# Optimization experiments

Measured on AMD Instinct MI355X. Metric: run time of the kernel, lower is better.

## Reference

```python
import jax, jax.numpy as jnp
import numpy as np

TOP_K = 128
HID = 256


def _mlp2(h, w1, b1, w2, b2):
    return jax.nn.relu(h @ w1 + b1) @ w2 + b2


def setup_inputs() -> dict:
    key = jax.random.key(0)
    ks = jax.random.split(key, 20)
    B, L, D = 512, 256, 64
    s = 0.05
    inp = {
        "x": jax.random.normal(ks[0], (B, L, D), dtype=jnp.float32),
        "Wq": jax.random.normal(ks[1], (D, HID)) * s, "bq": jnp.zeros((HID,)),
        "Wk": jax.random.normal(ks[2], (D, HID)) * s, "bk": jnp.zeros((HID,)),
        "phi_w1": jax.random.normal(ks[3], (D, HID)) * s, "phi_b1": jnp.zeros((HID,)),
        "phi_w2": jax.random.normal(ks[4], (HID, HID)) * s, "phi_b2": jnp.zeros((HID,)),
        "xi_w1": jax.random.normal(ks[5], (2 * D, HID)) * s, "xi_b1": jnp.zeros((HID,)),
        "xi_w2": jax.random.normal(ks[6], (HID, HID)) * s, "xi_b2": jnp.zeros((HID,)),
        "rho_w1": jax.random.normal(ks[7], (HID, HID)) * s, "rho_b1": jnp.zeros((HID,)),
        "rho_w2": jax.random.normal(ks[8], (HID, 128)) * s, "rho_b2": jnp.zeros((128,)),
    }
    return inp


def reference(x, Wq, bq, Wk, bk, phi_w1, phi_b1, phi_w2, phi_b2,
              xi_w1, xi_b1, xi_w2, xi_b2, rho_w1, rho_b1, rho_w2, rho_b2):
    B, L, D = x.shape
    scale = HID ** (-0.5)
    # padding mask (all True for randn input; trim is identity with static shapes)
    pad = jnp.sum(jnp.abs(x), axis=-1) != 0  # [B, L]
    Q = x @ Wq + bq  # [B, L, H]
    K = x @ Wk + bk
    scores = jnp.einsum("blh,bmh->blm", Q, K) * scale  # [B, L, L]
    mask2d = pad[:, :, None] & pad[:, None, :]
    scores = jnp.where(mask2d, scores, -jnp.inf)
    flat = scores.reshape(B, L * L)
    k = min(TOP_K, L * L)
    topk_vals, topk_idx = jax.lax.top_k(flat, k)  # [B, k]
    topk_w = jax.nn.softmax(topk_vals, axis=-1)
    row = topk_idx // L
    col = topk_idx % L
    x_i = jnp.take_along_axis(x, row[:, :, None], axis=1)  # [B, k, D]
    x_j = jnp.take_along_axis(x, col[:, :, None], axis=1)
    feat_self = _mlp2(x_i, phi_w1, phi_b1, phi_w2, phi_b2)  # [B, k, H]
    feat_pair = _mlp2(jnp.concatenate([x_i, x_j], axis=-1), xi_w1, xi_b1, xi_w2, xi_b2)
    self_mask = (row == col)[:, :, None]
    interaction = jnp.where(self_mask, feat_self, feat_pair)
    pooled = jnp.sum(interaction * topk_w[:, :, None], axis=1)  # [B, H]
    return _mlp2(pooled, rho_w1, rho_b1, rho_w2, rho_b2)  # [B, 128]
```

## Files before the change

kernel.cpp:

```cpp
#include <hip/hip_runtime.h>

typedef unsigned short u16;
typedef unsigned int   u32;
typedef unsigned char  u8;
typedef unsigned long long u64;

#define B_TOT 512
#define L_SEQ 256
#define D_IN  64
#define HIDN  256
#define TOPK  128
#define CAP   160
#define NWT   32
#define FLDS  113280

typedef float  f32x4  __attribute__((ext_vector_type(4)));
typedef __bf16 bf16x8 __attribute__((ext_vector_type(8)));

__device__ __forceinline__ u16 f2bf(float f){
  u32 u = __float_as_uint(f);
  u32 r = u + 0x7fffu + ((u>>16)&1u);
  return (u16)(r>>16);
}
__device__ __forceinline__ u32 sortKey(float f){
  u32 b = __float_as_uint(f);
  return (b & 0x80000000u) ? ~b : (b | 0x80000000u);
}
__device__ __forceinline__ float unKey(u32 u){
  u32 b = (u & 0x80000000u) ? (u & 0x7fffffffu) : ~u;
  return __uint_as_float(b);
}
__device__ __forceinline__ void cvt8(const float* v, u32* hp, u32* lp){
  #pragma unroll
  for (int i=0;i<4;++i){
    float v0 = v[2*i], v1 = v[2*i+1];
    u16 h0 = f2bf(v0); float h0f = __uint_as_float(((u32)h0)<<16); u16 l0 = f2bf(v0 - h0f);
    u16 h1 = f2bf(v1); float h1f = __uint_as_float(((u32)h1)<<16); u16 l1 = f2bf(v1 - h1f);
    hp[i] = (u32)h0 | ((u32)h1<<16);
    lp[i] = (u32)l0 | ((u32)l1<<16);
  }
}

__global__ __launch_bounds__(256) void k_wprep(
    const float* __restrict__ Wq, const float* __restrict__ bq,
    const float* __restrict__ Wk, const float* __restrict__ bk,
    const float* __restrict__ xi_w1, const float* __restrict__ phi_w1,
    u16* __restrict__ MtH, u16* __restrict__ MtL, float* __restrict__ uvc,
    u16* __restrict__ xiH, u16* __restrict__ xiL,
    u16* __restrict__ phiH, u16* __restrict__ phiL)
{
  int bid = blockIdx.x, tid = threadIdx.x;
  if (bid < 64){
    __shared__ float wq[HIDN];
    __shared__ float part[256];
    int a = bid;
    wq[tid] = Wq[a*HIDN + tid];
    __syncthreads();
    int bcol = tid & 63, q = tid >> 6;
    float s = 0.f;
    for (int h = q*64; h < q*64 + 64; ++h)
      s = fmaf(wq[h], Wk[bcol*HIDN + h], s);
    part[tid] = s;
    __syncthreads();
    if (tid < 64){
      float mv = part[tid] + part[64+tid] + part[128+tid] + part[192+tid];
      u16 hh = f2bf(mv); float hf = __uint_as_float(((u32)hh)<<16);
      u16 ll = f2bf(mv - hf);
      MtH[tid*64 + a] = hh;
      MtL[tid*64 + a] = ll;
    }
    int wv = tid >> 6, ln = tid & 63;
    if (wv == 0){
      float s2 = 0.f;
      #pragma unroll
      for (int i=0;i<4;++i){ int h = ln*4+i; s2 = fmaf(wq[h], bk[h], s2); }
      #pragma unroll
      for (int off=1; off<64; off<<=1) s2 += __shfl_xor(s2, off);
      if (ln == 0) uvc[a] = s2;
    } else if (wv == 1){
      float s2 = 0.f;
      #pragma unroll
      for (int i=0;i<4;++i){ int h = ln*4+i; s2 = fmaf(Wk[a*HIDN + h], bq[h], s2); }
      #pragma unroll
      for (int off=1; off<64; off<<=1) s2 += __shfl_xor(s2, off);
      if (ln == 0) uvc[64 + a] = s2;
    } else if (wv == 2 && a == 0){
      float s2 = 0.f;
      #pragma unroll
      for (int i=0;i<4;++i){ int h = ln*4+i; s2 = fmaf(bq[h], bk[h], s2); }
      #pragma unroll
      for (int off=1; off<64; off<<=1) s2 += __shfl_xor(s2, off);
      if (ln == 0) uvc[128] = s2;
    }
  } else {
    int t = (bid-64)*256 + tid;
    if (t < 256*128){
      int h = t >> 7, d = t & 127;
      float v = xi_w1[d*HIDN + h];
      u16 hh = f2bf(v); float hf = __uint_as_float(((u32)hh)<<16);
      u16 ll = f2bf(v - hf);
      xiH[h*128 + d] = hh; xiL[h*128 + d] = ll;
    } else {
      int t2 = t - 256*128;
      int h = t2 >> 6, d = t2 & 63;
      float v = phi_w1[d*HIDN + h];
      u16 hh = f2bf(v); float hf = __uint_as_float(((u32)hh)<<16);
      u16 ll = f2bf(v - hf);
      phiH[h*64 + d] = hh; phiL[h*64 + d] = ll;
    }
  }
}

__global__ __launch_bounds__(512) void k_fused(
    const float* __restrict__ x, const u16* __restrict__ MtH, const u16* __restrict__ MtL,
    const float* __restrict__ uvc,
    u64* __restrict__ cand, int* __restrict__ cand_n, u32* __restrict__ uthr)
{
  extern __shared__ __align__(16) u16 smem[];
  u16* XH = smem;
  u16* XL = XH + 256*72;
  u16* YH = XL + 256*72;
  u16* YL = YH + 128*72;
  float* STS = (float*)(YL + 128*72);
  float* STT = STS + 256;
  float* SUV = STT + 256;

  int tid = threadIdx.x;
  int b = blockIdx.x;
  const float* xb = x + (size_t)b*(L_SEQ*D_IN);

  if (tid < 129) SUV[tid] = uvc[tid];

  int ar = tid >> 1, ahf = tid & 1;
  float v[32];
  {
    const float* src = xb + (size_t)ar*D_IN + ahf*32;
    #pragma unroll
    for (int i=0;i<8;++i) *(float4*)&v[i*4] = *(const float4*)(src + i*4);
    u32 hp[16], lp[16];
    cvt8(&v[0],  &hp[0],  &lp[0]);
    cvt8(&v[8],  &hp[4],  &lp[4]);
    cvt8(&v[16], &hp[8],  &lp[8]);
    cvt8(&v[24], &hp[12], &lp[12]);
    u16* dh = XH + ar*72 + ahf*32;
    u16* dl = XL + ar*72 + ahf*32;
    #pragma unroll
    for (int i=0;i<4;++i){
      *(uint4*)(dh + i*8) = make_uint4(hp[i*4],hp[i*4+1],hp[i*4+2],hp[i*4+3]);
      *(uint4*)(dl + i*8) = make_uint4(lp[i*4],lp[i*4+1],lp[i*4+2],lp[i*4+3]);
    }
  }
  __syncthreads();

  {
    float pA=0.f, pB=0.f, qA=0.f, qB=0.f, pa=0.f;
    #pragma unroll
    for (int d=0; d<16; ++d){
      float xa = v[d];
      pA = fmaf(xa, SUV[ahf*32+d], pA);
      qA = fmaf(xa, SUV[64+ahf*32+d], qA);
      pa += fabsf(xa);
    }
    #pragma unroll
    for (int d=16; d<32; ++d){
      float xa = v[d];
      pB = fmaf(xa, SUV[ahf*32+d], pB);
      qB = fmaf(xa, SUV[64+ahf*32+d], qB);
      pa += fabsf(xa);
    }
    float su = pA + pB, tv = qA + qB;
    su += __shfl_xor(su,1); tv += __shfl_xor(tv,1); pa += __shfl_xor(pa,1);
    if (ahf == 0){
      bool pad = (pa != 0.f);
      STS[ar] = pad ? (su + SUV[128]) : -1e38f;
      STT[ar] = pad ? tv : -1e38f;
    }
  }
  __syncthreads();

  int w = tid >> 6, lane = tid & 63, lm = lane & 15, quad = lane >> 4;

  for (int half=0; half<2; ++half){
    int u = w + 8*half;
    int r0 = u*16;

    {
      const u16* ah = XH + (r0+lm)*72;
      const u16* al = XL + (r0+lm)*72;
      bf16x8 Ah0 = *(const bf16x8*)(ah + quad*8);
      bf16x8 Ah1 = *(const bf16x8*)(ah + 32 + quad*8);
      bf16x8 Al0 = *(const bf16x8*)(al + quad*8);
      bf16x8 Al1 = *(const bf16x8*)(al + 32 + quad*8);
      #pragma unroll
      for (int ct=0; ct<4; ++ct){
        const u16* mth = MtH + (ct*16+lm)*64 + quad*8;
        const u16* mtl = MtL + (ct*16+lm)*64 + quad*8;
        bf16x8 Bh0 = *(const bf16x8*)(mth);
        bf16x8 Bh1 = *(const bf16x8*)(mth + 32);
        bf16x8 Bl0 = *(const bf16x8*)(mtl);
        bf16x8 Bl1 = *(const bf16x8*)(mtl + 32);
        f32x4 a1 = {0.f,0.f,0.f,0.f}, a2 = {0.f,0.f,0.f,0.f};
        a1 = __builtin_amdgcn_mfma_f32_16x16x32_bf16(Ah0, Bh0, a1, 0,0,0);
        a2 = __builtin_amdgcn_mfma_f32_16x16x32_bf16(Ah1, Bh1, a2, 0,0,0);
        a1 = __builtin_amdgcn_mfma_f32_16x16x32_bf16(Al0, Bh0, a1, 0,0,0);
        a2 = __builtin_amdgcn_mfma_f32_16x16x32_bf16(Al1, Bh1, a2, 0,0,0);
        a1 = __builtin_amdgcn_mfma_f32_16x16x32_bf16(Ah0, Bl0, a1, 0,0,0);
        a2 = __builtin_amdgcn_mfma_f32_16x16x32_bf16(Ah1, Bl1, a2, 0,0,0);
        #pragma unroll
        for (int rg=0; rg<4; ++rg){
          float vy = a1[rg] + a2[rg];
          u16 hh = f2bf(vy); float hf = __uint_as_float(((u32)hh)<<16);
          u16 ll = f2bf(vy - hf);
          YH[(w*16 + quad*4 + rg)*72 + ct*16 + lm] = hh;
          YL[(w*16 + quad*4 + rg)*72 + ct*16 + lm] = ll;
        }
      }
    }
    const u16* yh_ = YH + (w*16+lm)*72;
    const u16* yl_ = YL + (w*16+lm)*72;
    bf16x8 Yh0 = *(const bf16x8*)(yh_ + quad*8);
    bf16x8 Yh1 = *(const bf16x8*)(yh_ + 32 + quad*8);
    bf16x8 Yl0 = *(const bf16x8*)(yl_ + quad*8);
    bf16x8 Yl1 = *(const bf16x8*)(yl_ + 32 + quad*8);

    float sr[4];
    #pragma unroll
    for (int r=0;r<4;++r) sr[r] = STS[r0 + quad*4 + r];

    for (int ch=0; ch<2; ++ch){
      int j0 = ch*128;
      u32 kv[32];
      #pragma unroll
      for (int ct=0; ct<8; ++ct){
        const u16* bh = XH + (j0 + ct*16+lm)*72;
        const u16* bl = XL + (j0 + ct*16+lm)*72;
        bf16x8 Bh0 = *(const bf16x8*)(bh + quad*8);
        bf16x8 Bh1 = *(const bf16x8*)(bh + 32 + quad*8);
        bf16x8 Bl0 = *(const bf16x8*)(bl + quad*8);
        bf16x8 Bl1 = *(const bf16x8*)(bl + 32 + quad*8);
        f32x4 a1 = {0.f,0.f,0.f,0.f}, a2 = {0.f,0.f,0.f,0.f};
        a1 = __builtin_amdgcn_mfma_f32_16x16x32_bf16(Yh0, Bh0, a1, 0,0,0);
        a2 = __builtin_amdgcn_mfma_f32_16x16x32_bf16(Yh1, Bh1, a2, 0,0,0);
        a1 = __builtin_amdgcn_mfma_f32_16x16x32_bf16(Yl0, Bh0, a1, 0,0,0);
        a2 = __builtin_amdgcn_mfma_f32_16x16x32_bf16(Yl1, Bh1, a2, 0,0,0);
        a1 = __builtin_amdgcn_mfma_f32_16x16x32_bf16(Yh0, Bl0, a1, 0,0,0);
        a2 = __builtin_amdgcn_mfma_f32_16x16x32_bf16(Yh1, Bl1, a2, 0,0,0);
        float tc = STT[j0 + ct*16 + lm];
        #pragma unroll
        for (int r=0;r<4;++r)
          kv[ct*4 + r] = sortKey(a1[r] + a2[r] + sr[r] + tc);
      }

      u32 T = 0;
      for (int bit=15; bit>=0; --bit){
        u32 th2 = (T | (1u<<bit)) << 16;
        int c0 = 0, c1 = 0;
        #pragma unroll
        for (int i=0;i<32;i+=2){
          c0 += (int)__popcll(__ballot(kv[i]   >= th2));
          c1 += (int)__popcll(__ballot(kv[i+1] >= th2));
        }
        int c = c0 + c1;
        if (c >= TOPK){
          T |= (1u<<bit);
          if (c <= CAP) break;
        }
      }
      u32 thr = T << 16;
      u32 up  = (T < 0xffffu) ? ((T+1u) << 16) : 0xffffffffu;

      u32 m1 = 0, m2 = 0;
      #pragma unroll
      for (int i=0;i<32;++i){
        bool ge = kv[i] >= thr;
        bool c1 = ge && (kv[i] >= up);
        m1 |= (c1 ? 1u : 0u) << i;
        m2 |= ((ge && !c1) ? 1u : 0u) << i;
      }
      int n1 = __popc(m1), n2 = __popc(m2);
      int p1 = n1, p2 = n2;
      #pragma unroll
      for (int off=1; off<64; off<<=1){
        int a = __shfl_up(p1, off); if (lane >= off) p1 += a;
        int c = __shfl_up(p2, off); if (lane >= off) p2 += c;
      }
      int tot1 = __shfl(p1, 63), tot2 = __shfl(p2, 63);
      int pos1 = p1 - n1;
      int pos2 = tot1 + (p2 - n2);
      int total = tot1 + tot2;
      int wt = u*2 + ch;
      size_t base = ((size_t)b*NWT + wt)*CAP;
      if (lane == 0){
        cand_n[b*NWT + wt] = (total < CAP) ? total : CAP;
        uthr[b*NWT + wt] = thr;
      }
      {
        int o1=0, o2=0;
        #pragma unroll
        for (int i=0;i<32;++i){
          bool c1 = (m1 >> i) & 1u, c2v = (m2 >> i) & 1u;
          if (c1 | c2v){
            int p = c1 ? (pos1 + o1) : (pos2 + o2);
            int flat = (r0 + quad*4 + (i&3))*L_SEQ + (j0 + (i>>2)*16 + lm);
            if (p < CAP) cand[base + p] = ((u64)kv[i] << 32) | (u32)flat;
          }
          o1 += c1; o2 += c2v;
        }
      }
    }
  }
}

__global__ __launch_bounds__(256) void k_pre(
    const float* __restrict__ x, const u16* __restrict__ MtH, const u16* __restrict__ MtL,
    const float* __restrict__ uvc,
    u16* __restrict__ xh, u16* __restrict__ xl,
    u16* __restrict__ yh, u16* __restrict__ yl,
    float* __restrict__ st)
{
  __shared__ __align__(16) u16 sh[64][72];
  __shared__ __align__(16) u16 sl[64][72];
  __shared__ float sUV[132];
  int tid = threadIdx.x;
  int g0 = blockIdx.x * 64;
  int b  = g0 >> 8, l0 = g0 & 255;
  int r = tid >> 2, q = tid & 3;

  if (tid < 129) sUV[tid] = uvc[tid];

  float v[16];
  {
    const float* xr = x + (size_t)(g0 + r)*D_IN + q*16;
    #pragma unroll
    for (int i=0;i<4;++i) *(float4*)&v[i*4] = *(const float4*)(xr + i*4);
  }
  {
    u32 hpA[4],lpA[4],hpB[4],lpB[4];
    cvt8(&v[0], hpA, lpA); cvt8(&v[8], hpB, lpB);
    size_t xo = (size_t)(g0 + r)*D_IN + q*16;
    *(uint4*)(xh + xo)     = make_uint4(hpA[0],hpA[1],hpA[2],hpA[3]);
    *(uint4*)(xh + xo + 8) = make_uint4(hpB[0],hpB[1],hpB[2],hpB[3]);
    *(uint4*)(xl + xo)     = make_uint4(lpA[0],lpA[1],lpA[2],lpA[3]);
    *(uint4*)(xl + xo + 8) = make_uint4(lpB[0],lpB[1],lpB[2],lpB[3]);
    *(uint4*)&sh[r][q*16]   = make_uint4(hpA[0],hpA[1],hpA[2],hpA[3]);
    *(uint4*)&sh[r][q*16+8] = make_uint4(hpB[0],hpB[1],hpB[2],hpB[3]);
    *(uint4*)&sl[r][q*16]   = make_uint4(lpA[0],lpA[1],lpA[2],lpA[3]);
    *(uint4*)&sl[r][q*16+8] = make_uint4(lpB[0],lpB[1],lpB[2],lpB[3]);
  }
  __syncthreads();

  {
    float su=0.f, tv=0.f, pa=0.f;
    #pragma unroll
    for (int d=0; d<16; ++d){
      float xa = v[d];
      su = fmaf(xa, sUV[q*16+d], su);
      tv = fmaf(xa, sUV[64+q*16+d], tv);
      pa += fabsf(xa);
    }
    su += __shfl_xor(su,1); su += __shfl_xor(su,2);
    tv += __shfl_xor(tv,1); tv += __shfl_xor(tv,2);
    pa += __shfl_xor(pa,1); pa += __shfl_xor(pa,2);
    if (q == 0){
      bool pad = (pa != 0.f);
      st[(size_t)b*L_SEQ + l0 + r]          = pad ? (su + sUV[128]) : -1e38f;
      st[(size_t)(B_TOT+b)*L_SEQ + l0 + r]  = pad ? tv : -1e38f;
    }
  }

  int w = tid >> 6, lane = tid & 63, lm = lane & 15, quad = lane >> 4;
  bf16x8 Ah0 = *(const bf16x8*)&sh[w*16+lm][quad*8];
  bf16x8 Ah1 = *(const bf16x8*)&sh[w*16+lm][32 + quad*8];
  bf16x8 Al0 = *(const bf16x8*)&sl[w*16+lm][quad*8];
  bf16x8 Al1 = *(const bf16x8*)&sl[w*16+lm][32 + quad*8];
  #pragma unroll
  for (int ct=0; ct<4; ++ct){
    const u16* mth = MtH + (ct*16+lm)*64 + quad*8;
    const u16* mtl = MtL + (ct*16+lm)*64 + quad*8;
    bf16x8 Bh0 = *(const bf16x8*)(mth);
    bf16x8 Bh1 = *(const bf16x8*)(mth + 32);
    bf16x8 Bl0 = *(const bf16x8*)(mtl);
    bf16x8 Bl1 = *(const bf16x8*)(mtl + 32);
    f32x4 a1 = {0.f,0.f,0.f,0.f}, a2 = {0.f,0.f,0.f,0.f};
    a1 = __builtin_amdgcn_mfma_f32_16x16x32_bf16(Ah0, Bh0, a1, 0,0,0);
    a2 = __builtin_amdgcn_mfma_f32_16x16x32_bf16(Ah1, Bh1, a2, 0,0,0);
    a1 = __builtin_amdgcn_mfma_f32_16x16x32_bf16(Al0, Bh0, a1, 0,0,0);
    a2 = __builtin_amdgcn_mfma_f32_16x16x32_bf16(Al1, Bh1, a2, 0,0,0);
    a1 = __builtin_amdgcn_mfma_f32_16x16x32_bf16(Ah0, Bl0, a1, 0,0,0);
    a2 = __builtin_amdgcn_mfma_f32_16x16x32_bf16(Ah1, Bl1, a2, 0,0,0);
    #pragma unroll
    for (int rg=0; rg<4; ++rg){
      float vy = a1[rg] + a2[rg];
      u16 hh = f2bf(vy); float hf = __uint_as_float(((u32)hh)<<16);
      u16 ll = f2bf(vy - hf);
      sh[w*16 + quad*4 + rg][ct*16 + lm] = hh;
      sl[w*16 + quad*4 + rg][ct*16 + lm] = ll;
    }
  }
  {
    size_t yo = (size_t)(g0 + r)*D_IN + q*16;
    *(uint4*)(yh + yo)     = *(uint4*)&sh[r][q*16];
    *(uint4*)(yh + yo + 8) = *(uint4*)&sh[r][q*16+8];
    *(uint4*)(yl + yo)     = *(uint4*)&sl[r][q*16];
    *(uint4*)(yl + yo + 8) = *(uint4*)&sl[r][q*16+8];
  }
}

__global__ __launch_bounds__(256) void k_score(
    const u16* __restrict__ xh, const u16* __restrict__ xl,
    const u16* __restrict__ yh, const u16* __restrict__ yl,
    const float* __restrict__ st,
    u64* __restrict__ cand, int* __restrict__ cand_n, u32* __restrict__ uthr)
{
  int tid = threadIdx.x;
  int lin = blockIdx.x;
  int b    = ((lin >> 6) << 3) | (lin & 7);
  int tile = (lin >> 3) & 7;
  int cb = tile & 1, rb = tile >> 1;
  int r0 = rb*64, j0 = cb*128;
  int w = tid >> 6, lane = tid & 63, lm = lane & 15, quad = lane >> 4;

  size_t rowA = ((size_t)b*L_SEQ + r0 + w*16 + lm)*D_IN;
  bf16x8 A_h0 = *(const bf16x8*)(yh + rowA + quad*8);
  bf16x8 A_h1 = *(const bf16x8*)(yh + rowA + 32 + quad*8);
  bf16x8 A_l0 = *(const bf16x8*)(yl + rowA + quad*8);
  bf16x8 A_l1 = *(const bf16x8*)(yl + rowA + 32 + quad*8);

  float4 s4 = *(const float4*)(st + (size_t)b*L_SEQ + r0 + w*16 + quad*4);
  float sr[4] = {s4.x, s4.y, s4.z, s4.w};
  float tc[8];
  #pragma unroll
  for (int ct=0;ct<8;++ct)
    tc[ct] = st[(size_t)(B_TOT + b)*L_SEQ + j0 + ct*16 + lm];

  u32 kv[32];
  #pragma unroll
  for (int ct=0; ct<8; ++ct){
    size_t rowB = ((size_t)b*L_SEQ + j0 + ct*16 + lm)*D_IN;
    bf16x8 B_h0 = *(const bf16x8*)(xh + rowB + quad*8);
    bf16x8 B_h1 = *(const bf16x8*)(xh + rowB + 32 + quad*8);
    bf16x8 B_l0 = *(const bf16x8*)(xl + rowB + quad*8);
    bf16x8 B_l1 = *(const bf16x8*)(xl + rowB + 32 + quad*8);
    f32x4 a1 = {0.f,0.f,0.f,0.f}, a2 = {0.f,0.f,0.f,0.f};
    a1 = __builtin_amdgcn_mfma_f32_16x16x32_bf16(A_h0, B_h0, a1, 0,0,0);
    a2 = __builtin_amdgcn_mfma_f32_16x16x32_bf16(A_h1, B_h1, a2, 0,0,0);
    a1 = __builtin_amdgcn_mfma_f32_16x16x32_bf16(A_l0, B_h0, a1, 0,0,0);
    a2 = __builtin_amdgcn_mfma_f32_16x16x32_bf16(A_l1, B_h1, a2, 0,0,0);
    a1 = __builtin_amdgcn_mfma_f32_16x16x32_bf16(A_h0, B_l0, a1, 0,0,0);
    a2 = __builtin_amdgcn_mfma_f32_16x16x32_bf16(A_h1, B_l1, a2, 0,0,0);
    #pragma unroll
    for (int r=0;r<4;++r)
      kv[ct*4 + r] = sortKey(a1[r] + a2[r] + sr[r] + tc[ct]);
  }

  u32 T = 0;
  for (int bit=15; bit>=0; --bit){
    u32 th2 = (T | (1u<<bit)) << 16;
    int c = 0;
    #pragma unroll
    for (int i=0;i<32;++i)
      c += (int)__popcll(__ballot(kv[i] >= th2));
    if (c >= TOPK){
      T |= (1u<<bit);
      if (c <= CAP) break;
    }
  }
  u32 thr = T << 16;

  u32 hm = 0;
  #pragma unroll
  for (int i=0;i<32;++i) hm |= (kv[i] >= thr ? 1u : 0u) << i;
  int myc = __popc(hm);
  int pre = myc;
  #pragma unroll
  for (int off=1; off<64; off<<=1){
    int n = __shfl_up(pre, off);
    if (lane >= off) pre += n;
  }
  int total = __shfl(pre, 63);
  int pos = pre - myc;
  int wt = tile*4 + w;
  size_t base = ((size_t)b*NWT + wt)*CAP;
  if (lane == 0){
    cand_n[b*NWT + wt] = (total < CAP) ? total : CAP;
    uthr[b*NWT + wt] = thr;
  }
  while (hm){
    int i = __ffs(hm) - 1; hm &= hm - 1;
    if (pos < CAP){
      int r = i & 3, ct = i >> 2;
      int flat = (r0 + w*16 + quad*4 + r)*L_SEQ + (j0 + ct*16 + lm);
      cand[base + pos] = ((u64)kv[i] << 32) | (u32)flat;
    }
    ++pos;
  }
}

__global__ __launch_bounds__(256) void k_merge(
    const u64* __restrict__ cand, const int* __restrict__ cand_n, const u32* __restrict__ uthr,
    int* __restrict__ selidx, float* __restrict__ selw)
{
  const int SL   = NWT/4;
  const int NSW  = SL*CAP/64;
  const int WCAP = 192;
  __shared__ u64 wbuf[4][WCAP];
  __shared__ int wcnt[4];
  __shared__ int scnt[NWT];
  __shared__ u32 wT[4];
  __shared__ int cm, eqc;
  __shared__ int eqi[256];
  __shared__ float sv[TOPK]; __shared__ int si[TOPK];
  __shared__ float fred[8];
  int b = blockIdx.x, tid = threadIdx.x;
  int w = tid >> 6, lane = tid & 63;
  if (tid < NWT) scnt[tid] = cand_n[b*NWT + tid];
  if (tid == 0){ cm = 0; eqc = 0; }
  __syncthreads();

  u32 key[NSW]; int idx[NSW];
  size_t bb = (size_t)b*NWT*CAP + (size_t)(w*SL)*CAP;
  #pragma unroll
  for (int s=0;s<NSW;++s){
    int e = lane + 64*s;
    int slot = e / CAP, p = e - slot*CAP;
    bool ok = p < scnt[w*SL + slot];
    u64 v = ok ? cand[bb + e] : 0ull;
    key[s] = (u32)(v >> 32);
    idx[s] = ok ? (int)(u32)v : 0x7fffffff;
  }

  u32 lb = uthr[b*NWT + w*SL + (lane & 7)];
  #pragma unroll
  for (int off=1; off<8; off<<=1){
    u32 o = (u32)__shfl_xor((int)lb, off);
    lb = lb > o ? lb : o;
  }

  u32 T = 0;
  for (int bit=31; bit>=0; --bit){
    u32 c2 = T | (1u<<bit);
    if (c2 <= lb){ T = c2; continue; }
    int c = 0;
    #pragma unroll
    for (int s=0;s<NSW;++s) c += (int)__popcll(__ballot(key[s] >= c2));
    if (c >= TOPK){
      T = c2;
      if (c <= WCAP) break;
    }
  }
  if (lane == 0) wT[w] = T;
  {
    int myc = 0;
    #pragma unroll
    for (int s=0;s<NSW;++s) myc += (key[s] >= T) ? 1 : 0;
    int pre = myc;
    #pragma unroll
    for (int off=1; off<64; off<<=1){
      int n = __shfl_up(pre, off);
      if (lane >= off) pre += n;
    }
    int total = __shfl(pre, 63);
    int pos = pre - myc;
    if (lane == 0) wcnt[w] = (total < WCAP) ? total : WCAP;
    #pragma unroll
    for (int s=0;s<NSW;++s){
      if (key[s] >= T){
        if (pos < WCAP) wbuf[w][pos] = ((u64)key[s] << 32) | (u32)idx[s];
        ++pos;
      }
    }
  }
  __syncthreads();

  if (w == 0){
    const int NS2 = 4*WCAP/64;
    u32 k2[NS2]; int i2[NS2];
    #pragma unroll
    for (int s=0;s<NS2;++s){
      int e = lane + 64*s;
      int slot = e / WCAP, p = e - slot*WCAP;
      bool ok = p < wcnt[slot];
      u64 v = ok ? wbuf[slot][p] : 0ull;
      k2[s] = (u32)(v >> 32);
      i2[s] = ok ? (int)(u32)v : 0x7fffffff;
    }
    u32 lb2 = wT[0];
    lb2 = lb2 > wT[1] ? lb2 : wT[1];
    lb2 = lb2 > wT[2] ? lb2 : wT[2];
    lb2 = lb2 > wT[3] ? lb2 : wT[3];
    u32 T2 = 0;
    for (int bit=31; bit>=0; --bit){
      u32 c2 = T2 | (1u<<bit);
      if (c2 <= lb2){ T2 = c2; continue; }
      int c = 0;
      #pragma unroll
      for (int s=0;s<NS2;++s) c += (int)__popcll(__ballot(k2[s] >= c2));
      if (c >= TOPK) T2 = c2;
    }
    int m = 0;
    #pragma unroll
    for (int s=0;s<NS2;++s) m += (int)__popcll(__ballot(k2[s] > T2));
    #pragma unroll
    for (int s=0;s<NS2;++s){
      if (k2[s] > T2){
        int p = atomicAdd(&cm, 1);
        sv[p] = unKey(k2[s]) * 0.0625f; si[p] = i2[s];
      } else if (k2[s] == T2 && i2[s] != 0x7fffffff){
        int q = atomicAdd(&eqc, 1);
        if (q < 256) eqi[q] = i2[s];
      }
    }
    if (lane == 0){
      int need = TOPK - m;
      int n = eqc < 256 ? eqc : 256;
      float tv = unKey(T2) * 0.0625f;
      for (int s2=0; s2<need; ++s2){
        int bi = s2;
        for (int j=s2+1;j<n;++j) if (eqi[j] < eqi[bi]) bi = j;
        int t2 = eqi[s2]; eqi[s2] = eqi[bi]; eqi[bi] = t2;
        sv[m+s2] = tv; si[m+s2] = eqi[s2];
      }
    }
  }
  __syncthreads();

  float v = (tid < TOPK) ? sv[tid] : -3.4e38f;
  float mx = v;
  #pragma unroll
  for (int off=1; off<64; off<<=1) mx = fmaxf(mx, __shfl_xor(mx, off));
  if ((tid&63)==0) fred[tid>>6] = mx;
  __syncthreads();
  mx = fmaxf(fred[0], fred[1]);
  float e = (tid < TOPK) ? expf(v - mx) : 0.f;
  float s = e;
  #pragma unroll
  for (int off=1; off<64; off<<=1) s += __shfl_xor(s, off);
  if ((tid&63)==0) fred[4 + (tid>>6)] = s;
  __syncthreads();
  s = fred[4] + fred[5];
  if (tid < TOPK){
    selw[(size_t)b*TOPK + tid]   = e / s;
    selidx[(size_t)b*TOPK + tid] = si[tid];
  }
}

__global__ __launch_bounds__(256) void k_mlp(
    const float* __restrict__ x, const int* __restrict__ selidx, const float* __restrict__ selw,
    const u16* __restrict__ xiH, const u16* __restrict__ xiL,
    const u16* __restrict__ phiH, const u16* __restrict__ phiL,
    const float* __restrict__ phi_b1, const float* __restrict__ phi_w2, const float* __restrict__ phi_b2,
    const float* __restrict__ xi_b1,  const float* __restrict__ xi_w2,  const float* __restrict__ xi_b2,
    const float* __restrict__ rho_w1, const float* __restrict__ rho_b1,
    const float* __restrict__ rho_w2, const float* __restrict__ rho_b2,
    float* __restrict__ out)
{
  __shared__ __align__(16) u16 AFh[8][4][64][8];
  __shared__ __align__(16) u16 AFl[8][4][64][8];
  __shared__ int   sidx[TOPK];
  __shared__ float swp[TOPK], swd[TOPK];
  __shared__ float gpL[256], gsL[256];
  __shared__ float pooled[256], t1[256];
  __shared__ float wsums[2];
  int b = blockIdx.x, tid = threadIdx.x;

  if (tid < TOPK){
    int fl = selidx[(size_t)b*TOPK + tid];
    sidx[tid] = fl;
    float wv = selw[(size_t)b*TOPK + tid];
    bool dg = ((fl>>8) == (fl&255));
    swp[tid] = dg ? 0.f : wv;
    swd[tid] = dg ? wv  : 0.f;
  }
  __syncthreads();
  if (tid == 0){
    float a=0.f, c2=0.f;
    for (int k=0;k<TOPK;++k){ a+=swp[k]; c2+=swd[k]; }
    wsums[0]=a; wsums[1]=c2;
  }
  {
    int m = tid >> 1, hf = tid & 1;
    int fl = sidx[m];
    int rc = hf ? (fl & 255) : (fl >> 8);
    const float* src = x + ((size_t)b*L_SEQ + rc)*D_IN;
    int kt = m >> 4, l16 = m & 15;
    #pragma unroll
    for (int g=0; g<8; ++g){
      int d0 = hf*64 + g*8;
      int c = d0 >> 5, q = (d0 >> 3) & 3;
      float v[8];
      *(float4*)&v[0] = *(const float4*)(src + (d0 & 63));
      *(float4*)&v[4] = *(const float4*)(src + (d0 & 63) + 4);
      u32 hp[4], lp[4];
      cvt8(v, hp, lp);
      *(uint4*)&AFh[kt][c][l16 + 16*q][0] = make_uint4(hp[0],hp[1],hp[2],hp[3]);
      *(uint4*)&AFl[kt][c][l16 + 16*q][0] = make_uint4(lp[0],lp[1],lp[2],lp[3]);
    }
  }
  __syncthreads();

  int w = tid >> 6, lane = tid & 63;
  int lm = lane & 15, quad = lane >> 4;

  #pragma unroll
  for (int hi4=0; hi4<4; ++hi4){
    int ht = w + 4*hi4;
    int h  = ht*16 + lm;
    bf16x8 BXh[4], BXl[4], BPh[2], BPl[2];
    #pragma unroll
    for (int c=0;c<4;++c){
      BXh[c] = *(const bf16x8*)(xiH + h*128 + c*32 + quad*8);
      BXl[c] = *(const bf16x8*)(xiL + h*128 + c*32 + quad*8);
    }
    #pragma unroll
    for (int c=0;c<2;++c){
      BPh[c] = *(const bf16x8*)(phiH + h*64 + c*32 + quad*8);
      BPl[c] = *(const bf16x8*)(phiL + h*64 + c*32 + quad*8);
    }
    float bxi = xi_b1[h], bph = phi_b1[h];
    float gp = 0.f, gs = 0.f;
    for (int kt=0; kt<8; ++kt){
      bf16x8 Ah_[4], Al_[4];
      #pragma unroll
      for (int c=0;c<4;++c){
        Ah_[c] = *(const bf16x8*)&AFh[kt][c][lane][0];
        Al_[c] = *(const bf16x8*)&AFl[kt][c][lane][0];
      }
      f32x4 cx = {0.f,0.f,0.f,0.f}, cp = {0.f,0.f,0.f,0.f};
      #pragma unroll
      for (int c=0;c<4;++c){
        cx = __builtin_amdgcn_mfma_f32_16x16x32_bf16(Ah_[c], BXh[c], cx, 0,0,0);
        cx = __builtin_amdgcn_mfma_f32_16x16x32_bf16(Al_[c], BXh[c], cx, 0,0,0);
        cx = __builtin_amdgcn_mfma_f32_16x16x32_bf16(Ah_[c], BXl[c], cx, 0,0,0);
      }
      #pragma unroll
      for (int c=0;c<2;++c){
        cp = __builtin_amdgcn_mfma_f32_16x16x32_bf16(Ah_[c], BPh[c], cp, 0,0,0);
        cp = __builtin_amdgcn_mfma_f32_16x16x32_bf16(Al_[c], BPh[c], cp, 0,0,0);
        cp = __builtin_amdgcn_mfma_f32_16x16x32_bf16(Ah_[c], BPl[c], cp, 0,0,0);
      }
      #pragma unroll
      for (int r=0;r<4;++r){
        int kk = kt*16 + quad*4 + r;
        gp = fmaf(swp[kk], fmaxf(cx[r] + bxi, 0.f), gp);
        gs = fmaf(swd[kk], fmaxf(cp[r] + bph, 0.f), gs);
      }
    }
    gp += __shfl_xor(gp, 16); gp += __shfl_xor(gp, 32);
    gs += __shfl_xor(gs, 16); gs += __shfl_xor(gs, 32);
    if (quad == 0){ gpL[h] = gp; gsL[h] = gs; }
  }
  __syncthreads();

  int h = tid;
  {
    float wsp = wsums[0], wss = wsums[1];
    float po = wsp*xi_b2[h] + wss*phi_b2[h];
    for (int d=0; d<256; ++d){
      po = fmaf(gpL[d], xi_w2[d*HIDN + h], po);
      po = fmaf(gsL[d], phi_w2[d*HIDN + h], po);
    }
    pooled[h] = po;
  }
  __syncthreads();
  {
    float a = rho_b1[h];
    for (int d=0; d<256; ++d) a = fmaf(pooled[d], rho_w1[d*HIDN + h], a);
    t1[h] = fmaxf(a, 0.f);
  }
  __syncthreads();
  if (h < 128){
    float o = rho_b2[h];
    for (int d=0; d<256; ++d) o = fmaf(t1[d], rho_w2[d*128 + h], o);
    out[(size_t)b*128 + h] = o;
  }
}

extern "C" void kernel_launch(void* const* d_in, const int* in_sizes, int n_in,
                              void* d_out, int out_size, void* d_ws, size_t ws_size,
                              hipStream_t stream)
{
  (void)in_sizes; (void)n_in; (void)out_size; (void)ws_size;
  const float* x      = (const float*)d_in[0];
  const float* Wq     = (const float*)d_in[1];
  const float* bq     = (const float*)d_in[2];
  const float* Wk     = (const float*)d_in[3];
  const float* bk     = (const float*)d_in[4];
  const float* phi_w1 = (const float*)d_in[5];
  const float* phi_b1 = (const float*)d_in[6];
  const float* phi_w2 = (const float*)d_in[7];
  const float* phi_b2 = (const float*)d_in[8];
  const float* xi_w1  = (const float*)d_in[9];
  const float* xi_b1  = (const float*)d_in[10];
  const float* xi_w2  = (const float*)d_in[11];
  const float* xi_b2  = (const float*)d_in[12];
  const float* rho_w1 = (const float*)d_in[13];
  const float* rho_b1 = (const float*)d_in[14];
  const float* rho_w2 = (const float*)d_in[15];
  const float* rho_b2 = (const float*)d_in[16];
  float* out = (float*)d_out;

  const size_t NX = (size_t)B_TOT*L_SEQ*D_IN;
  float* uvc    = (float*)d_ws;
  float* st     = uvc + 256;
  float* selw   = st + (size_t)2*B_TOT*L_SEQ;
  int*   selidx = (int*)(selw + (size_t)B_TOT*TOPK);
  int*   cand_n = selidx + (size_t)B_TOT*TOPK;
  u32*   uthr   = (u32*)(cand_n + (size_t)B_TOT*NWT);
  u64*   cand   = (u64*)(uthr + (size_t)B_TOT*NWT);
  u16*   MtH    = (u16*)(cand + (size_t)B_TOT*NWT*CAP);
  u16*   MtL    = MtH + 64*64;
  u16*   xiH    = MtL + 64*64;
  u16*   xiL    = xiH + 256*128;
  u16*   phiH   = xiL + 256*128;
  u16*   phiL   = phiH + 256*64;
  u16*   xh     = phiL + 256*64;
  u16*   xl     = xh + NX;
  u16*   yh     = xl + NX;
  u16*   yl     = yh + NX;

  hipError_t aerr = hipFuncSetAttribute((const void*)k_fused,
                      hipFuncAttributeMaxDynamicSharedMemorySize, FLDS);

  k_wprep<<<dim3(256),  dim3(256), 0, stream>>>(Wq, bq, Wk, bk, xi_w1, phi_w1,
                                                MtH, MtL, uvc, xiH, xiL, phiH, phiL);
  if (aerr == hipSuccess){
    k_fused<<<dim3(B_TOT), dim3(512), FLDS, stream>>>(x, MtH, MtL, uvc, cand, cand_n, uthr);
  } else {
    k_pre  <<<dim3(2048), dim3(256), 0, stream>>>(x, MtH, MtL, uvc, xh, xl, yh, yl, st);
    k_score<<<dim3(4096), dim3(256), 0, stream>>>(xh, xl, yh, yl, st, cand, cand_n, uthr);
  }
  k_merge<<<dim3(B_TOT), dim3(256), 0, stream>>>(cand, cand_n, uthr, selidx, selw);
  k_mlp  <<<dim3(B_TOT), dim3(256), 0, stream>>>(x, selidx, selw,
            xiH, xiL, phiH, phiL,
            phi_b1, phi_w2, phi_b2,
            xi_b1, xi_w2, xi_b2,
            rho_w1, rho_b1, rho_w2, rho_b2, out);
}
```

Before: 265.5 us.

## Keep Y=X·M product in registers via transposed MFMA and permuted rows

```diff
diff --git a/kernel.cpp b/kernel.cpp
--- a/kernel.cpp
+++ b/kernel.cpp
@@ -12,7 +12,7 @@
 #define TOPK  128
 #define CAP   160
 #define NWT   32
-#define FLDS  113280
+#define FLDS  76304
 
 typedef float  f32x4  __attribute__((ext_vector_type(4)));
 typedef __bf16 bf16x8 __attribute__((ext_vector_type(8)));
@@ -111,7 +111,7 @@
   }
 }
 
-__global__ __launch_bounds__(512) void k_fused(
+__global__ __launch_bounds__(512, 4) void k_fused(
     const float* __restrict__ x, const u16* __restrict__ MtH, const u16* __restrict__ MtL,
     const float* __restrict__ uvc,
     u64* __restrict__ cand, int* __restrict__ cand_n, u32* __restrict__ uthr)
@@ -119,9 +119,7 @@
   extern __shared__ __align__(16) u16 smem[];
   u16* XH = smem;
   u16* XL = XH + 256*72;
-  u16* YH = XL + 256*72;
-  u16* YL = YH + 128*72;
-  float* STS = (float*)(YL + 128*72);
+  float* STS = (float*)(XL + 256*72);
   float* STT = STS + 256;
   float* SUV = STT + 256;
 
@@ -184,44 +182,52 @@
     int u = w + 8*half;
     int r0 = u*16;
 
+    bf16x8 Yh0, Yh1, Yl0, Yl1;
     {
-      const u16* ah = XH + (r0+lm)*72;
-      const u16* al = XL + (r0+lm)*72;
-      bf16x8 Ah0 = *(const bf16x8*)(ah + quad*8);
-      bf16x8 Ah1 = *(const bf16x8*)(ah + 32 + quad*8);
-      bf16x8 Al0 = *(const bf16x8*)(al + quad*8);
-      bf16x8 Al1 = *(const bf16x8*)(al + 32 + quad*8);
+      const u16* xh_ = XH + (r0+lm)*72;
+      const u16* xl_ = XL + (r0+lm)*72;
+      bf16x8 Xh0 = *(const bf16x8*)(xh_ + quad*8);
+      bf16x8 Xh1 = *(const bf16x8*)(xh_ + 32 + quad*8);
+      bf16x8 Xl0 = *(const bf16x8*)(xl_ + quad*8);
+      bf16x8 Xl1 = *(const bf16x8*)(xl_ + 32 + quad*8);
+      u32 yh[8], yl[8];
       #pragma unroll
       for (int ct=0; ct<4; ++ct){
-        const u16* mth = MtH + (ct*16+lm)*64 + quad*8;
-        const u16* mtl = MtL + (ct*16+lm)*64 + quad*8;
-        bf16x8 Bh0 = *(const bf16x8*)(mth);
-        bf16x8 Bh1 = *(const bf16x8*)(mth + 32);
-        bf16x8 Bl0 = *(const bf16x8*)(mtl);
-        bf16x8 Bl1 = *(const bf16x8*)(mtl + 32);
+        int srow = 8*(lm>>2) + 4*(ct&1) + (lm&3) + 32*(ct>>1);
+        const u16* mth = MtH + srow*64 + quad*8;
+        const u16* mtl = MtL + srow*64 + quad*8;
+        bf16x8 Mh0 = *(const bf16x8*)(mth);
+        bf16x8 Mh1 = *(const bf16x8*)(mth + 32);
+        bf16x8 Ml0 = *(const bf16x8*)(mtl);
+        bf16x8 Ml1 = *(const bf16x8*)(mtl + 32);
         f32x4 a1 = {0.f,0.f,0.f,0.f}, a2 = {0.f,0.f,0.f,0.f};
-        a1 = __builtin_amdgcn_mfma_f32_16x16x32_bf16(Ah0, Bh0, a1, 0,0,0);
-        a2 = __builtin_amdgcn_mfma_f32_16x16x32_bf16(Ah1, Bh1, a2, 0,0,0);
-        a1 = __builtin_amdgcn_mfma_f32_16x16x32_bf16(Al0, Bh0, a1, 0,0,0);
-        a2 = __builtin_amdgcn_mfma_f32_16x16x32_bf16(Al1, Bh1, a2, 0,0,0);
-        a1 = __builtin_amdgcn_mfma_f32_16x16x32_bf16(Ah0, Bl0, a1, 0,0,0);
-        a2 = __builtin_amdgcn_mfma_f32_16x16x32_bf16(Ah1, Bl1, a2, 0,0,0);
+        a1 = __builtin_amdgcn_mfma_f32_16x16x32_bf16(Mh0, Xh0, a1, 0,0,0);
+        a2 = __builtin_amdgcn_mfma_f32_16x16x32_bf16(Mh1, Xh1, a2, 0,0,0);
+        a1 = __builtin_amdgcn_mfma_f32_16x16x32_bf16(Ml0, Xh0, a1, 0,0,0);
+        a2 = __builtin_amdgcn_mfma_f32_16x16x32_bf16(Ml1, Xh1, a2, 0,0,0);
+        a1 = __builtin_amdgcn_mfma_f32_16x16x32_bf16(Mh0, Xl0, a1, 0,0,0);
+        a2 = __builtin_amdgcn_mfma_f32_16x16x32_bf16(Mh1, Xl1, a2, 0,0,0);
         #pragma unroll
-        for (int rg=0; rg<4; ++rg){
-          float vy = a1[rg] + a2[rg];
-          u16 hh = f2bf(vy); float hf = __uint_as_float(((u32)hh)<<16);
-          u16 ll = f2bf(vy - hf);
-          YH[(w*16 + quad*4 + rg)*72 + ct*16 + lm] = hh;
-          YL[(w*16 + quad*4 + rg)*72 + ct*16 + lm] = ll;
+        for (int pr=0; pr<2; ++pr){
+          float v0 = a1[2*pr]   + a2[2*pr];
+          float v1 = a1[2*pr+1] + a2[2*pr+1];
+          u16 h0 = f2bf(v0); u16 h1 = f2bf(v1);
+          u16 l0 = f2bf(v0 - __uint_as_float(((u32)h0)<<16));
+          u16 l1 = f2bf(v1 - __uint_as_float(((u32)h1)<<16));
+          int slot = (ct>>1)*4 + (ct&1)*2 + pr;
+          yh[slot] = (u32)h0 | ((u32)h1<<16);
+          yl[slot] = (u32)l0 | ((u32)l1<<16);
         }
       }
-    }
-    const u16* yh_ = YH + (w*16+lm)*72;
-    const u16* yl_ = YL + (w*16+lm)*72;
-    bf16x8 Yh0 = *(const bf16x8*)(yh_ + quad*8);
-    bf16x8 Yh1 = *(const bf16x8*)(yh_ + 32 + quad*8);
-    bf16x8 Yl0 = *(const bf16x8*)(yl_ + quad*8);
-    bf16x8 Yl1 = *(const bf16x8*)(yl_ + 32 + quad*8);
+      uint4 t0 = make_uint4(yh[0],yh[1],yh[2],yh[3]);
+      uint4 t1 = make_uint4(yh[4],yh[5],yh[6],yh[7]);
+      uint4 t2 = make_uint4(yl[0],yl[1],yl[2],yl[3]);
+      uint4 t3 = make_uint4(yl[4],yl[5],yl[6],yl[7]);
+      Yh0 = *(const bf16x8*)&t0;
+      Yh1 = *(const bf16x8*)&t1;
+      Yl0 = *(const bf16x8*)&t2;
+      Yl1 = *(const bf16x8*)&t3;
+    }
 
     float sr[4];
     #pragma unroll
```

Measured after the change: 276.1 us. 1.04x slower.
